# Kernel optimization log

Hardware: AMD Instinct MI355X
Metric: run time of the kernel (lower is better)

Reference implementation:

```python
import jax, jax.numpy as jnp
import numpy as np
from numpy.polynomial import Polynomial

EXP_START, EXP_STOP, EXP_N, EXP_DEG = -5.0, 5.0, 1000, 8
INV_START, INV_STOP, INV_N, INV_DEG = 1000.0, 6000.0, 1000, 4


def _ls_fit_coeffs(fn, start, stop, n, deg):
    # least-squares polynomial fit, converted to power basis (matches torch module)
    xs = np.linspace(start, stop, n)
    return Polynomial.fit(xs, fn(xs), deg).convert(kind=Polynomial).coef


def _horner(coeffs, x):
    # coeffs[k] is the coefficient of x**k (power basis); evaluate via Horner
    acc = jnp.full_like(x, coeffs[-1])
    for k in range(coeffs.shape[0] - 2, -1, -1):
        acc = acc * x + coeffs[k]
    return acc


def setup_inputs() -> dict:
    key = jax.random.key(0)
    x = jax.random.normal(key, (16, 2048, 2048), dtype=jnp.float32)
    exp_coeffs = jnp.asarray(_ls_fit_coeffs(np.exp, EXP_START, EXP_STOP, EXP_N, EXP_DEG), dtype=jnp.float32)
    inverse_coeffs = jnp.asarray(_ls_fit_coeffs(lambda t: 1.0 / t, INV_START, INV_STOP, INV_N, INV_DEG), dtype=jnp.float32)
    return {"x": x, "exp_coeffs": exp_coeffs, "inverse_coeffs": inverse_coeffs, "iterations": 3}


def reference(x, exp_coeffs, inverse_coeffs, iterations):
    # CKKS-style softmax: polynomial exp, row-sum, polynomial initial inverse,
    # Newton-Raphson reciprocal refinement, broadcast multiply.
    e = _horner(exp_coeffs, x)                      # [B, S, S] approx exp(x)
    s = jnp.sum(e, axis=-1, keepdims=True)          # [B, S, 1]
    y = _horner(inverse_coeffs, s)                  # initial guess for 1/s
    for _ in range(iterations):                     # Newton: y <- y*(2 - s*y)
        y = y * (2.0 - s * y)
    return e * y
```

## Files before the change

kernel.cpp:

```cpp
#include <hip/hip_runtime.h>


#define ROWLEN 2048
#define TPB    256

__global__ __launch_bounds__(TPB) void ckks_softmax_kernel(
    const float* __restrict__ x,
    const float* __restrict__ exp_c,
    const float* __restrict__ inv_c,
    const int*   __restrict__ iters_p,
    float* __restrict__ out)
{
    const int row = blockIdx.x;
    const int tid = threadIdx.x;
    const size_t base = (size_t)row * ROWLEN;

    const float4* __restrict__ xv = (const float4*)(x + base);
    float4* __restrict__ ov       = (float4*)(out + base);

    const float c0 = exp_c[0], c1 = exp_c[1], c2 = exp_c[2], c3 = exp_c[3],
                c4 = exp_c[4], c5 = exp_c[5], c6 = exp_c[6], c7 = exp_c[7],
                c8 = exp_c[8];

    float4 a = xv[tid];
    float4 b = xv[tid + TPB];

    auto horner8 = [&](float v) -> float {
        float acc = c8;
        acc = fmaf(acc, v, c7);
        acc = fmaf(acc, v, c6);
        acc = fmaf(acc, v, c5);
        acc = fmaf(acc, v, c4);
        acc = fmaf(acc, v, c3);
        acc = fmaf(acc, v, c2);
        acc = fmaf(acc, v, c1);
        acc = fmaf(acc, v, c0);
        return acc;
    };

    float4 ea, eb;
    ea.x = horner8(a.x); ea.y = horner8(a.y); ea.z = horner8(a.z); ea.w = horner8(a.w);
    eb.x = horner8(b.x); eb.y = horner8(b.y); eb.z = horner8(b.z); eb.w = horner8(b.w);

    float local = ((ea.x + ea.y) + (ea.z + ea.w)) + ((eb.x + eb.y) + (eb.z + eb.w));
    #pragma unroll
    for (int off = 32; off > 0; off >>= 1)
        local += __shfl_down(local, off, 64);

    __shared__ float wsum[TPB / 64];
    const int wave = tid >> 6;
    if ((tid & 63) == 0) wsum[wave] = local;
    __syncthreads();
    const float s = (wsum[0] + wsum[1]) + (wsum[2] + wsum[3]);

    float y = inv_c[4];
    y = fmaf(y, s, inv_c[3]);
    y = fmaf(y, s, inv_c[2]);
    y = fmaf(y, s, inv_c[1]);
    y = fmaf(y, s, inv_c[0]);

    const int iters = *iters_p;
    for (int i = 0; i < iters; ++i)
        y = y * (2.0f - s * y);

    ea.x *= y; ea.y *= y; ea.z *= y; ea.w *= y;
    eb.x *= y; eb.y *= y; eb.z *= y; eb.w *= y;

    ov[tid]       = ea;
    ov[tid + TPB] = eb;
}

extern "C" void kernel_launch(void* const* d_in, const int* in_sizes, int n_in,
                              void* d_out, int out_size, void* d_ws, size_t ws_size,
                              hipStream_t stream) {
    const float* x     = (const float*)d_in[0];
    const float* exp_c = (const float*)d_in[1];
    const float* inv_c = (const float*)d_in[2];
    const int*   iters = (const int*)d_in[3];
    float* out = (float*)d_out;

    const int n_rows = out_size / ROWLEN;
    ckks_softmax_kernel<<<n_rows, TPB, 0, stream>>>(x, exp_c, inv_c, iters, out);
}
```

Baseline: 430.7 us.

## Map each row to one wave with wave-only reduction and nontemporal memory ops

Each wavefront now handles a whole row, with four rows per block, so the row sum needs only xor shuffles and no shared memory or block barrier. Each lane loads eight vectors up front, giving more loads in flight. Loads and stores use nontemporal hints so the streaming data skips cache. Register use per thread goes up, which could lower occupancy.

```diff
diff --git a/kernel.cpp b/kernel.cpp
--- a/kernel.cpp
+++ b/kernel.cpp
@@ -1,8 +1,11 @@
 #include <hip/hip_runtime.h>
 
 
+typedef float v4f __attribute__((ext_vector_type(4)));
+
 #define ROWLEN 2048
 #define TPB    256
+#define ROWS_PER_BLOCK 4
 
 __global__ __launch_bounds__(TPB) void ckks_softmax_kernel(
     const float* __restrict__ x,
@@ -11,63 +14,70 @@
     const int*   __restrict__ iters_p,
     float* __restrict__ out)
 {
-    const int row = blockIdx.x;
-    const int tid = threadIdx.x;
+    const int lane = threadIdx.x & 63;
+    const int wave = threadIdx.x >> 6;
+    const int row  = blockIdx.x * ROWS_PER_BLOCK + wave;
     const size_t base = (size_t)row * ROWLEN;
 
-    const float4* __restrict__ xv = (const float4*)(x + base);
-    float4* __restrict__ ov       = (float4*)(out + base);
+    const v4f* __restrict__ xv = (const v4f*)(x + base);
+    v4f*       __restrict__ ov = (v4f*)(out + base);
 
     const float c0 = exp_c[0], c1 = exp_c[1], c2 = exp_c[2], c3 = exp_c[3],
                 c4 = exp_c[4], c5 = exp_c[5], c6 = exp_c[6], c7 = exp_c[7],
                 c8 = exp_c[8];
+    const float i0 = inv_c[0], i1 = inv_c[1], i2 = inv_c[2], i3 = inv_c[3],
+                i4 = inv_c[4];
+    const int iters = *iters_p;
 
-    float4 a = xv[tid];
-    float4 b = xv[tid + TPB];
+    v4f v[8];
+    #pragma unroll
+    for (int k = 0; k < 8; ++k)
+        v[k] = __builtin_nontemporal_load(&xv[lane + 64 * k]);
 
-    auto horner8 = [&](float v) -> float {
+    auto horner8 = [&](float t) -> float {
         float acc = c8;
-        acc = fmaf(acc, v, c7);
-        acc = fmaf(acc, v, c6);
-        acc = fmaf(acc, v, c5);
-        acc = fmaf(acc, v, c4);
-        acc = fmaf(acc, v, c3);
-        acc = fmaf(acc, v, c2);
-        acc = fmaf(acc, v, c1);
-        acc = fmaf(acc, v, c0);
+        acc = fmaf(acc, t, c7);
+        acc = fmaf(acc, t, c6);
+        acc = fmaf(acc, t, c5);
+        acc = fmaf(acc, t, c4);
+        acc = fmaf(acc, t, c3);
+        acc = fmaf(acc, t, c2);
+        acc = fmaf(acc, t, c1);
+        acc = fmaf(acc, t, c0);
         return acc;
     };
 
-    float4 ea, eb;
-    ea.x = horner8(a.x); ea.y = horner8(a.y); ea.z = horner8(a.z); ea.w = horner8(a.w);
-    eb.x = horner8(b.x); eb.y = horner8(b.y); eb.z = horner8(b.z); eb.w = horner8(b.w);
+    v4f acc4 = {0.0f, 0.0f, 0.0f, 0.0f};
+    #pragma unroll
+    for (int k = 0; k < 8; ++k) {
+        v4f e;
+        e.x = horner8(v[k].x);
+        e.y = horner8(v[k].y);
+        e.z = horner8(v[k].z);
+        e.w = horner8(v[k].w);
+        v[k] = e;
+        acc4 += e;
+    }
+    float s = (acc4.x + acc4.y) + (acc4.z + acc4.w);
 
-    float local = ((ea.x + ea.y) + (ea.z + ea.w)) + ((eb.x + eb.y) + (eb.z + eb.w));
     #pragma unroll
     for (int off = 32; off > 0; off >>= 1)
-        local += __shfl_down(local, off, 64);
+        s += __shfl_xor(s, off, 64);
 
-    __shared__ float wsum[TPB / 64];
-    const int wave = tid >> 6;
-    if ((tid & 63) == 0) wsum[wave] = local;
-    __syncthreads();
-    const float s = (wsum[0] + wsum[1]) + (wsum[2] + wsum[3]);
+    float y = i4;
+    y = fmaf(y, s, i3);
+    y = fmaf(y, s, i2);
+    y = fmaf(y, s, i1);
+    y = fmaf(y, s, i0);
 
-    float y = inv_c[4];
-    y = fmaf(y, s, inv_c[3]);
-    y = fmaf(y, s, inv_c[2]);
-    y = fmaf(y, s, inv_c[1]);
-    y = fmaf(y, s, inv_c[0]);
-
-    const int iters = *iters_p;
     for (int i = 0; i < iters; ++i)
         y = y * (2.0f - s * y);
 
-    ea.x *= y; ea.y *= y; ea.z *= y; ea.w *= y;
-    eb.x *= y; eb.y *= y; eb.z *= y; eb.w *= y;
-
-    ov[tid]       = ea;
-    ov[tid + TPB] = eb;
+    #pragma unroll
+    for (int k = 0; k < 8; ++k) {
+        v4f e = v[k] * y;
+        __builtin_nontemporal_store(e, &ov[lane + 64 * k]);
+    }
 }
 
 extern "C" void kernel_launch(void* const* d_in, const int* in_sizes, int n_in,
@@ -80,5 +90,6 @@
     float* out = (float*)d_out;
 
     const int n_rows = out_size / ROWLEN;
-    ckks_softmax_kernel<<<n_rows, TPB, 0, stream>>>(x, exp_c, inv_c, iters, out);
+    const int n_blocks = n_rows / ROWS_PER_BLOCK;
+    ckks_softmax_kernel<<<n_blocks, TPB, 0, stream>>>(x, exp_c, inv_c, iters, out);
 }
```

Result: no change. 424.1 us (-1.5%).
